# Kernel tuning notes

Hardware: AMD Instinct MI355X
Metric: run time of the kernel (lower is better)

Reference implementation:

```python
import jax, jax.numpy as jnp
import numpy as np
from jax import lax

NEG = jnp.float32(-1e30)  # log-domain 'zero'
BLANK = 0


def setup_inputs() -> dict:
    T, N, C, S = 512, 512, 80, 128
    k0, k1, k2, k3 = jax.random.split(jax.random.key(0), 4)
    logits = jax.random.normal(k0, (T, N, C), dtype=jnp.float32)
    log_probs = jax.nn.log_softmax(logits, axis=-1)  # CTCLoss expects log-probs
    targets = jax.random.randint(k1, (N, S), 1, C).astype(jnp.int32)  # labels in [1, C-1], blank=0 excluded
    input_lengths = jax.random.randint(k2, (N,), T // 2, T + 1).astype(jnp.int32)
    target_lengths = jax.random.randint(k3, (N,), S // 2, S + 1).astype(jnp.int32)
    return {"log_probs": log_probs, "targets": targets,
            "input_lengths": input_lengths, "target_lengths": target_lengths}


def _ctc_loss(log_probs, targets, input_lengths, target_lengths):
    # log_probs: (T, N, C) log-probabilities; targets: (N, S) labels (no blanks)
    T, N, C = log_probs.shape
    S = targets.shape[1]
    L = 2 * S + 1  # extended label length: blank-interleaved

    # extended targets: [blank, y1, blank, y2, ..., yS, blank]  -> (N, L)
    ext = jnp.zeros((N, L), jnp.int32).at[:, 1::2].set(targets)
    # skip transition (s-2 -> s) allowed only if ext[s] != ext[s-2]
    # (blank positions have ext[s]==ext[s-2]==blank, so this also forbids blank skips)
    skip_ok = jnp.pad(ext[:, 2:] != ext[:, :-2], ((0, 0), (2, 0)), constant_values=False)

    # emission log-probs on the lattice: (T, N, L)
    emit = jnp.take_along_axis(log_probs, jnp.broadcast_to(ext[None], (T, N, L)), axis=2)

    # alpha at t=0: only lattice positions 0 (blank) and 1 (first label) reachable
    alpha0 = jnp.full((N, L), NEG).at[:, 0].set(emit[0, :, 0]).at[:, 1].set(emit[0, :, 1])

    def step(alpha, xs):
        em, t = xs  # em: (N, L)
        a1 = jnp.pad(alpha[:, :-1], ((0, 0), (1, 0)), constant_values=NEG)
        a2 = jnp.where(skip_ok,
                       jnp.pad(alpha[:, :-2], ((0, 0), (2, 0)), constant_values=NEG), NEG)
        m = jnp.maximum(alpha, jnp.maximum(a1, a2))
        lse = m + jnp.log(jnp.exp(alpha - m) + jnp.exp(a1 - m) + jnp.exp(a2 - m))
        new = lse + em
        # freeze alpha for finished sequences (t >= input_length)
        alpha_new = jnp.where((t < input_lengths)[:, None], new, alpha)
        return alpha_new, None

    alpha_T, _ = lax.scan(step, alpha0, (emit[1:], jnp.arange(1, T, dtype=jnp.int32)))

    # final states: last blank (2*tl) and last label (2*tl - 1)
    i1 = (2 * target_lengths)[:, None]
    v1 = jnp.take_along_axis(alpha_T, i1, axis=1)[:, 0]
    v2 = jnp.take_along_axis(alpha_T, i1 - 1, axis=1)[:, 0]
    m = jnp.maximum(v1, v2)
    loss = -(m + jnp.log(jnp.exp(v1 - m) + jnp.exp(v2 - m)))
    # zero_infinity=True: infeasible alignments -> 0 loss
    loss = jnp.where(jnp.isfinite(loss) & (loss < 1e10), loss, 0.0)
    return loss  # (N,) reduction='none'


def reference(log_probs, targets, input_lengths, target_lengths):
    return _ctc_loss(log_probs, targets, input_lengths, target_lengths)
```

## Files before the change

### kernel.cpp

```cpp
#include <hip/hip_runtime.h>


#define NEGC  (-1.0e30f)
#define LOG2E 1.4426950408889634f
#define LN2   0.6931471805599453f

constexpr int T_ = 512;
constexpr int C_ = 80;
constexpr int S_ = 128;
constexpr int U_ = 8;
constexpr int WROW = 520;

__device__ __forceinline__ float exp2a(float x) { return __builtin_amdgcn_exp2f(x); }
__device__ __forceinline__ float log2a(float x) { return __builtin_amdgcn_logf(x); }

template <int CTRL>
__device__ __forceinline__ float dppf(float old_, float src) {
    return __int_as_float(__builtin_amdgcn_update_dpp(
        __float_as_int(old_), __float_as_int(src), CTRL, 0xF, 0xF, false));
}

__device__ __forceinline__ int wave_max_bits(float m) {
    m = fmaxf(m, dppf<0x111>(m, m));
    m = fmaxf(m, dppf<0x112>(m, m));
    m = fmaxf(m, dppf<0x114>(m, m));
    m = fmaxf(m, dppf<0x118>(m, m));
    m = fmaxf(m, dppf<0x142>(m, m));
    m = fmaxf(m, dppf<0x143>(m, m));
    return __builtin_amdgcn_readlane(__float_as_int(m), 63);
}

__device__ __forceinline__ float lse2(float x, float y) {
    float m = fmaxf(x, y);
    return m + log2a(1.0f + exp2a(-fabsf(x - y)));
}
__device__ __forceinline__ float lse3(float x, float y, float z) {
    float m = fmaxf(x, fmaxf(y, z));
    return m + log2a(exp2a(x - m) + exp2a(y - m) + exp2a(z - m));
}

__global__ __launch_bounds__(64, 1) void ctc_half(
    const float* __restrict__ lp, const int* __restrict__ tgt,
    const int* __restrict__ ilen, const int* __restrict__ tlen,
    float* __restrict__ ws, int N)
{
    const int b   = blockIdx.x;
    const int n   = b >> 1;
    const int dir = b & 1;
    const int l   = threadIdx.x;

    __shared__ float lds[1280];

    float* ga = ws + (size_t)n * WROW;
    float* gg = ga + 260;

    const int* tn = tgt + n * S_;
    const int ext1 = tn[2 * l];
    const int ext3 = tn[2 * l + 1];
    const int prev = (l > 0) ? tn[2 * l - 1] : 0;
    const bool skip1 = (l > 0) && (ext1 != prev);
    const bool skip3 = (ext3 != ext1);
    const bool skb3  = (l < 63) && (tn[2 * l + 2] != ext3);
    const float k1f  = skip1 ? 1.0f : 0.0f;
    const float k3f  = skip3 ? 1.0f : 0.0f;
    const float kb3f = skb3  ? 1.0f : 0.0f;

    int len = ilen[n];
    len = len < 1 ? 1 : (len > T_ ? T_ : len);
    const int mid = len >> 1;

    const int irst = N * C_;
    const float* lpn = lp + (size_t)n * C_;

    int dkr[10], ckk[10];
    #pragma unroll
    for (int k = 0; k < 10; ++k) {
        const unsigned flat = (unsigned)l + 64u * k;
        const unsigned dk = flat / 80u;
        ckk[k] = (int)(flat - 80u * dk);
        dkr[k] = (int)dk * irst;
    }

    float VA[10], VB[10];
    float ebA[8], e1A[8], e3A[8];
    float ebB[8], e1B[8], e3B[8];

#define SISSUE_F(FB, V) do {                                                   \
    const int s_ = (FB) * irst;                                                \
    _Pragma("unroll")                                                          \
    for (int k = 0; k < 10; ++k)                                               \
        V[k] = lpn[(unsigned)(s_ + dkr[k] + ckk[k])];                          \
} while (0)

#define SISSUE_B(FB, V) do {                                                   \
    const int s_ = (FB) * irst;                                                \
    _Pragma("unroll")                                                          \
    for (int k = 0; k < 10; ++k) {                                             \
        int v_ = s_ - dkr[k]; v_ = v_ < 0 ? 0 : v_;                            \
        V[k] = lpn[(unsigned)(v_ + ckk[k])];                                   \
    }                                                                          \
} while (0)

#define SWRITE(H, V) do {                                                      \
    _Pragma("unroll")                                                          \
    for (int k = 0; k < 10; ++k)                                               \
        lds[(H) * 640 + l + 64 * k] = exp2a(V[k] * LOG2E);                     \
} while (0)

#define RLOAD(H, EB, E1, E3) do {                                              \
    _Pragma("unroll")                                                          \
    for (int u = 0; u < 8; ++u) {                                              \
        const int base_ = (H) * 640 + u * 80;                                  \
        EB[u] = lds[base_];                                                    \
        E1[u] = lds[base_ + ext1];                                             \
        E3[u] = lds[base_ + ext3];                                             \
    }                                                                          \
} while (0)

#define RENORM(S0, S1, S2, S3, S4) do {                                        \
    const int mi_ = wave_max_bits(                                             \
        fmaxf(fmaxf(fmaxf(S0, S1), fmaxf(S2, S3)), S4));                       \
    const int e_ = (mi_ > 0) ? (((mi_ >> 23) & 255) - 187) : 0;                \
    E += e_;                                                                   \
    S0 = ldexpf(S0, -e_); S1 = ldexpf(S1, -e_); S2 = ldexpf(S2, -e_);          \
    S3 = ldexpf(S3, -e_); S4 = ldexpf(S4, -e_);                                \
} while (0)

#define COMP8_F(TB, CEB, CE1, CE3, RH, NEB, NE1, NE3) do {                     \
    _Pragma("unroll")                                                          \
    for (int u = 0; u < 8; ++u) {                                              \
        const int t_ = (TB) + u;                                               \
        const int rb_ = (RH) * 640 + u * 80;                                   \
        NEB[u] = lds[rb_]; NE1[u] = lds[rb_ + ext1]; NE3[u] = lds[rb_ + ext3]; \
        if (t_ < mid) {                                                        \
            const float Pb_ = CEB[u], Q1_ = CE1[u], Q3_ = CE3[u];              \
            const float sm1_ = dppf<0x138>(0.0f, p3_);      \
            const float i0_ = p0_ + sm1_;                                      \
            const float i1_ = fmaf(sm1_, k1f, p1_ + p0_);                      \
            const float i2_ = p2_ + p1_;                                       \
            const float i3_ = fmaf(p1_, k3f, p3_ + p2_);                       \
            const float i4_ = p4_ + p3_;                                       \
            p0_ = i0_ * Pb_; p1_ = i1_ * Q1_; p2_ = i2_ * Pb_;                 \
            p3_ = i3_ * Q3_; p4_ = i4_ * Pb_;                                  \
        }                                                                      \
    }                                                                          \
} while (0)

#define COMP8_B(TB, CEB, CE1, CE3, RH, NEB, NE1, NE3) do {                     \
    _Pragma("unroll")                                                          \
    for (int u = 0; u < 8; ++u) {                                              \
        const int t_ = (TB) - u;                                               \
        const int rb_ = (RH) * 640 + u * 80;                                   \
        NEB[u] = lds[rb_]; NE1[u] = lds[rb_ + ext1]; NE3[u] = lds[rb_ + ext3]; \
        if (t_ >= mid) {                                                       \
            const float Pb_ = CEB[u], Q1_ = CE1[u], Q3_ = CE3[u];              \
            const float x0_ = dppf<0x130>(g4_, g0_);    \
            const float x1_ = dppf<0x130>(0.f, g1_);    \
            const float i0_ = g0_ + g1_;                                       \
            const float i1_ = fmaf(g3_, k3f, g1_ + g2_);                       \
            const float i2_ = g2_ + g3_;                                       \
            const float i3_ = fmaf(x1_, kb3f, g3_ + x0_);                      \
            g0_ = i0_ * Pb_; g1_ = i1_ * Q1_; g2_ = i2_ * Pb_;                 \
            g3_ = i3_ * Q3_; g4_ = g4_ * Pb_;                                  \
        }                                                                      \
    }                                                                          \
} while (0)

    if (dir == 0) {
        SISSUE_F(1, VA);  SISSUE_F(9, VB);
        SWRITE(0, VA);    SWRITE(1, VB);
        SISSUE_F(17, VA); SISSUE_F(25, VB);
        RLOAD(0, ebA, e1A, e3A);

        float p0_ = 0.f, p1_ = 0.f, p2_ = 0.f, p3_ = 0.f, p4_ = 0.f;
        int   E = -60;
        if (l == 0) {
            p0_ = exp2a(lpn[0] * LOG2E + 60.0f);
            p1_ = exp2a(lpn[ext1] * LOG2E + 60.0f);
        }
        for (int tb = 1; tb < mid; tb += 16) {
            COMP8_F(tb, ebA, e1A, e3A, 1, ebB, e1B, e3B);
            RENORM(p0_, p1_, p2_, p3_, p4_);
            SWRITE(0, VA);
            SISSUE_F(tb + 32, VA);
            COMP8_F(tb + 8, ebB, e1B, e3B, 0, ebA, e1A, e3A);
            RENORM(p0_, p1_, p2_, p3_, p4_);
            SWRITE(1, VB);
            SISSUE_F(tb + 40, VB);
        }
        const float fE = (float)E;
        ga[4 * l + 0] = (p0_ > 0.f) ? fmaxf(log2a(p0_) + fE, NEGC) : NEGC;
        ga[4 * l + 1] = (p1_ > 0.f) ? fmaxf(log2a(p1_) + fE, NEGC) : NEGC;
        ga[4 * l + 2] = (p2_ > 0.f) ? fmaxf(log2a(p2_) + fE, NEGC) : NEGC;
        ga[4 * l + 3] = (p3_ > 0.f) ? fmaxf(log2a(p3_) + fE, NEGC) : NEGC;
        if (l == 63) ga[256] = (p4_ > 0.f) ? fmaxf(log2a(p4_) + fE, NEGC) : NEGC;
    } else {
        const int fe = len - 1;
        SISSUE_B(fe - 1, VA);  SISSUE_B(fe - 9, VB);
        SWRITE(0, VA);         SWRITE(1, VB);
        SISSUE_B(fe - 17, VA); SISSUE_B(fe - 25, VB);
        RLOAD(0, ebA, e1A, e3A);

        const int tl = tlen[n];
        const int sA = 2 * tl, sB = 2 * tl - 1;
        float g0_, g1_, g2_, g3_, g4_;
        int E = -60;
        {
            const unsigned feo = (unsigned)(fe * irst);
            const float ebi = lpn[feo] * LOG2E + 60.0f;
            const float e1i = lpn[feo + ext1] * LOG2E + 60.0f;
            const float e3i = lpn[feo + ext3] * LOG2E + 60.0f;
            const int s0 = 4 * l;
            g0_ = (s0     == sA)                 ? exp2a(ebi) : 0.f;
            g1_ = (s0 + 1 == sA || s0 + 1 == sB) ? exp2a(e1i) : 0.f;
            g2_ = (s0 + 2 == sA)                 ? exp2a(ebi) : 0.f;
            g3_ = (s0 + 3 == sA || s0 + 3 == sB) ? exp2a(e3i) : 0.f;
            g4_ = (l == 63 && 256 == sA)         ? exp2a(ebi) : 0.f;
        }
        for (int tb = fe - 1; tb >= mid; tb -= 16) {
            COMP8_B(tb, ebA, e1A, e3A, 1, ebB, e1B, e3B);
            RENORM(g0_, g1_, g2_, g3_, g4_);
            SWRITE(0, VA);
            SISSUE_B(tb - 32, VA);
            COMP8_B(tb - 8, ebB, e1B, e3B, 0, ebA, e1A, e3A);
            RENORM(g0_, g1_, g2_, g3_, g4_);
            SWRITE(1, VB);
            SISSUE_B(tb - 40, VB);
        }
        const float fE = (float)E;
        gg[4 * l + 0] = (g0_ > 0.f) ? fmaxf(log2a(g0_) + fE, NEGC) : NEGC;
        gg[4 * l + 1] = (g1_ > 0.f) ? fmaxf(log2a(g1_) + fE, NEGC) : NEGC;
        gg[4 * l + 2] = (g2_ > 0.f) ? fmaxf(log2a(g2_) + fE, NEGC) : NEGC;
        gg[4 * l + 3] = (g3_ > 0.f) ? fmaxf(log2a(g3_) + fE, NEGC) : NEGC;
        if (l == 63) gg[256] = (g4_ > 0.f) ? fmaxf(log2a(g4_) + fE, NEGC) : NEGC;
    }
#undef COMP8_F
#undef COMP8_B
#undef SISSUE_F
#undef SISSUE_B
#undef SWRITE
#undef RLOAD
#undef RENORM
}

__global__ __launch_bounds__(64) void ctc_comb(
    const float* __restrict__ ws, const int* __restrict__ tgt,
    const int* __restrict__ ilen, const int* __restrict__ tlen,
    float* __restrict__ out, int N)
{
    const int n = blockIdx.x;
    const int l = threadIdx.x;
    const float* ga = ws + (size_t)n * WROW;
    const float* gg = ga + 260;

    int len = ilen[n];
    len = len < 1 ? 1 : (len > T_ ? T_ : len);
    const int tl = tlen[n];

    if (len == 1) {
        if (l == 0) {
            const float v1 = ga[2 * tl];
            const float v2 = (2 * tl >= 1) ? ga[2 * tl - 1] : NEGC;
            float loss = -lse2(v1, v2) * LN2;
            if (!(loss < 1e10f) || !isfinite(loss)) loss = 0.0f;
            out[n] = loss;
        }
        return;
    }

    const int* tn = tgt + n * S_;
    const int ext1 = tn[2 * l];
    const int ext3 = tn[2 * l + 1];
    const int prev = (l > 0) ? tn[2 * l - 1] : 0;
    const bool skip1 = (l > 0) && (ext1 != prev);
    const bool skip3 = (ext3 != ext1);

    const int s0 = 4 * l;
    const float Am1 = (l > 0) ? ga[s0 - 1] : NEGC;
    const float A0 = ga[s0], A1 = ga[s0 + 1], A2 = ga[s0 + 2], A3 = ga[s0 + 3];
    const float v0 = lse2(A0, Am1)                    + gg[s0];
    const float v1 = lse3(A1, A0, skip1 ? Am1 : NEGC) + gg[s0 + 1];
    const float v2 = lse2(A2, A1)                     + gg[s0 + 2];
    const float v3 = lse3(A3, A2, skip3 ? A1 : NEGC)  + gg[s0 + 3];
    const float v4 = (l == 63) ? (lse2(ga[256], A3) + gg[256]) : NEGC;

    float m = fmaxf(fmaxf(v0, v1), fmaxf(fmaxf(v2, v3), v4));
    float ssum = exp2a(v0 - m) + exp2a(v1 - m) + exp2a(v2 - m)
               + exp2a(v3 - m) + exp2a(v4 - m);
    float M = m;
    #pragma unroll
    for (int d = 1; d < 64; d <<= 1) M = fmaxf(M, __shfl_xor(M, d));
    float r = ssum * exp2a(m - M);
    #pragma unroll
    for (int d = 1; d < 64; d <<= 1) r += __shfl_xor(r, d);
    if (l == 0) {
        float loss = -LN2 * (M + log2a(r));
        if (!(loss < 1e10f) || !isfinite(loss)) loss = 0.0f;
        out[n] = loss;
    }
}

__global__ __launch_bounds__(128) void ctc_fused(
    const float* __restrict__ lp, const int* __restrict__ tgt,
    const int* __restrict__ ilen, const int* __restrict__ tlen,
    float* __restrict__ out, int N)
{
    const int n    = blockIdx.x;
    const int wave = threadIdx.x >> 6;
    const int l    = threadIdx.x & 63;

    __shared__ float ga[2 * S_ + 1];
    __shared__ float gg[2 * S_ + 1];

    const int* tn = tgt + n * S_;
    const int ext1 = tn[2 * l];
    const int ext3 = tn[2 * l + 1];
    const int prev = (l > 0) ? tn[2 * l - 1] : 0;
    const bool skip1 = (l > 0) && (ext1 != prev);
    const bool skip3 = (ext3 != ext1);
    const bool skb1 = (tn[2 * l + 1] != tn[2 * l]);
    const bool skb3 = (l < 63) && (tn[2 * l + 2] != tn[2 * l + 1]);

    int len = ilen[n];
    len = len < 1 ? 1 : (len > T_ ? T_ : len);
    const int mid = len >> 1;

    const size_t rstride = (size_t)N * C_;
    const float* lpn = lp + (size_t)n * C_;
    const float* pB = lpn;
    const float* p1 = lpn + ext1;
    const float* p3 = lpn + ext3;

    float rb[U_], r1[U_], r3[U_];

    if (wave == 0) {
        const int last = mid - 1 > 0 ? mid - 1 : 0;
        #pragma unroll
        for (int u = 0; u < U_; ++u) {
            const int r = u + 1;
            const int rc = r < mid ? r : last;
            const size_t o = (size_t)rc * rstride;
            rb[r & 7] = pB[o]; r1[r & 7] = p1[o]; r3[r & 7] = p3[o];
        }
        float a0 = NEGC, a1 = NEGC, a2 = NEGC, a3 = NEGC, a4 = NEGC;
        {
            const float i0 = pB[0] * LOG2E;
            const float i1 = p1[0] * LOG2E;
            if (l == 0) { a0 = i0; a1 = i1; }
        }
        for (int tb = 1; tb < mid; tb += U_) {
            #pragma unroll
            for (int u = 0; u < U_; ++u) {
                const int t = tb + u;
                const int slot = (1 + u) & 7;
                const float eb = rb[slot] * LOG2E;
                const float e1 = r1[slot] * LOG2E;
                const float e3 = r3[slot] * LOG2E;
                const int rr = t + U_;
                const int rc = rr < mid ? rr : last;
                const size_t o = (size_t)rc * rstride;
                const float nrb = pB[o], nr1 = p1[o], nr3 = p3[o];
                if (t < mid) {
                    const float sm1 = dppf<0x138>(NEGC, a3);
                    const float z1 = skip1 ? sm1 : NEGC;
                    const float z3 = skip3 ? a1  : NEGC;
                    const float n0 = lse2(a0, sm1)    + eb;
                    const float n1 = lse3(a1, a0, z1) + e1;
                    const float n2 = lse2(a2, a1)     + eb;
                    const float n3 = lse3(a3, a2, z3) + e3;
                    const float n4 = lse2(a4, a3)     + eb;
                    a0 = n0; a1 = n1; a2 = n2; a3 = n3; a4 = n4;
                }
                rb[slot] = nrb; r1[slot] = nr1; r3[slot] = nr3;
            }
        }
        ga[4 * l + 0] = a0; ga[4 * l + 1] = a1;
        ga[4 * l + 2] = a2; ga[4 * l + 3] = a3;
        if (l == 63) ga[256] = a4;
    } else {
        const int fe = len - 1;
        #pragma unroll
        for (int u = 0; u < U_; ++u) {
            int rc = fe - 1 - u; if (rc < 0) rc = 0;
            const size_t o = (size_t)rc * rstride;
            rb[u] = pB[o]; r1[u] = p1[o]; r3[u] = p3[o];
        }
        const int tl = tlen[n];
        const int sA = 2 * tl, sB = 2 * tl - 1;
        float g0, g1, g2, g3, g4;
        {
            const size_t o = (size_t)fe * rstride;
            const float ebi = pB[o] * LOG2E;
            const float e1i = p1[o] * LOG2E;
            const float e3i = p3[o] * LOG2E;
            const int s0 = 4 * l;
            g0 = (s0     == sA)                 ? ebi : NEGC;
            g1 = (s0 + 1 == sA || s0 + 1 == sB) ? e1i : NEGC;
            g2 = (s0 + 2 == sA)                 ? ebi : NEGC;
            g3 = (s0 + 3 == sA || s0 + 3 == sB) ? e3i : NEGC;
            g4 = (l == 63 && 256 == sA)         ? ebi : NEGC;
        }
        for (int tb = fe - 1; tb >= mid; tb -= U_) {
            #pragma unroll
            for (int u = 0; u < U_; ++u) {
                const int t = tb - u;
                const int slot = ((fe - 1 - tb) + u) & 7;
                const float eb = rb[slot] * LOG2E;
                const float e1 = r1[slot] * LOG2E;
                const float e3 = r3[slot] * LOG2E;
                int rc = t - U_; if (rc < 0) rc = 0;
                const size_t o = (size_t)rc * rstride;
                const float nrb = pB[o], nr1 = p1[o], nr3 = p3[o];
                if (t >= mid) {
                    const float nx0 = dppf<0x130>(g4,   g0);
                    const float nx1 = dppf<0x130>(NEGC, g1);
                    const float z1 = skb1 ? g3  : NEGC;
                    const float z3 = skb3 ? nx1 : NEGC;
                    const float n0 = lse2(g0, g1)      + eb;
                    const float n1 = lse3(g1, g2, z1)  + e1;
                    const float n2 = lse2(g2, g3)      + eb;
                    const float n3 = lse3(g3, nx0, z3) + e3;
                    const float n4 = g4 + eb;
                    g0 = n0; g1 = n1; g2 = n2; g3 = n3; g4 = n4;
                }
                rb[slot] = nrb; r1[slot] = nr1; r3[slot] = nr3;
            }
        }
        gg[4 * l + 0] = g0; gg[4 * l + 1] = g1;
        gg[4 * l + 2] = g2; gg[4 * l + 3] = g3;
        if (l == 63) gg[256] = g4;
    }

    __syncthreads();

    if (wave == 0) {
        const int tl = tlen[n];
        if (len == 1) {
            if (l == 0) {
                const float v1 = ga[2 * tl];
                const float v2 = (2 * tl >= 1) ? ga[2 * tl - 1] : NEGC;
                float loss = -lse2(v1, v2) * LN2;
                if (!(loss < 1e10f) || !isfinite(loss)) loss = 0.0f;
                out[n] = loss;
            }
            return;
        }
        const int s0 = 4 * l;
        const float Am1 = (l > 0) ? ga[s0 - 1] : NEGC;
        const float A0 = ga[s0], A1 = ga[s0 + 1], A2 = ga[s0 + 2], A3 = ga[s0 + 3];
        const float v0 = lse2(A0, Am1)                    + gg[s0];
        const float v1 = lse3(A1, A0, skip1 ? Am1 : NEGC) + gg[s0 + 1];
        const float v2 = lse2(A2, A1)                     + gg[s0 + 2];
        const float v3 = lse3(A3, A2, skip3 ? A1 : NEGC)  + gg[s0 + 3];
        const float v4 = (l == 63) ? (lse2(ga[256], A3) + gg[256]) : NEGC;

        float m = fmaxf(fmaxf(v0, v1), fmaxf(fmaxf(v2, v3), v4));
        float ssum = exp2a(v0 - m) + exp2a(v1 - m) + exp2a(v2 - m)
                   + exp2a(v3 - m) + exp2a(v4 - m);
        float M = m;
        #pragma unroll
        for (int d = 1; d < 64; d <<= 1) M = fmaxf(M, __shfl_xor(M, d));
        float r = ssum * exp2a(m - M);
        #pragma unroll
        for (int d = 1; d < 64; d <<= 1) r += __shfl_xor(r, d);
        if (l == 0) {
            float loss = -LN2 * (M + log2a(r));
            if (!(loss < 1e10f) || !isfinite(loss)) loss = 0.0f;
            out[n] = loss;
        }
    }
}

extern "C" void kernel_launch(void* const* d_in, const int* in_sizes, int n_in,
                              void* d_out, int out_size, void* d_ws, size_t ws_size,
                              hipStream_t stream) {
    const float* lp  = (const float*)d_in[0];
    const int*   tg  = (const int*)  d_in[1];
    const int*   il  = (const int*)  d_in[2];
    const int*   tl  = (const int*)  d_in[3];
    float*       out = (float*)d_out;
    const int N = in_sizes[2];
    const size_t need = (size_t)N * WROW * sizeof(float);
    if (ws_size >= need) {
        ctc_half<<<2 * N, 64, 0, stream>>>(lp, tg, il, tl, (float*)d_ws, N);
        ctc_comb<<<N, 64, 0, stream>>>((const float*)d_ws, tg, il, tl, out, N);
    } else {
        ctc_fused<<<N, 128, 0, stream>>>(lp, tg, il, tl, out, N);
    }
}
```

Before: 133.1 us.

## Fuse forward/backward halves and combine into one two-wave block per sequence

```diff
diff --git a/kernel.cpp b/kernel.cpp
--- a/kernel.cpp
+++ b/kernel.cpp
@@ -8,8 +8,6 @@
 constexpr int T_ = 512;
 constexpr int C_ = 80;
 constexpr int S_ = 128;
-constexpr int U_ = 8;
-constexpr int WROW = 520;
 
 __device__ __forceinline__ float exp2a(float x) { return __builtin_amdgcn_exp2f(x); }
 __device__ __forceinline__ float log2a(float x) { return __builtin_amdgcn_logf(x); }
@@ -39,20 +37,19 @@
     return m + log2a(exp2a(x - m) + exp2a(y - m) + exp2a(z - m));
 }
 
-__global__ __launch_bounds__(64, 1) void ctc_half(
+__global__ __launch_bounds__(128, 1) void ctc_all(
     const float* __restrict__ lp, const int* __restrict__ tgt,
     const int* __restrict__ ilen, const int* __restrict__ tlen,
-    float* __restrict__ ws, int N)
+    float* __restrict__ out, int N)
 {
-    const int b   = blockIdx.x;
-    const int n   = b >> 1;
-    const int dir = b & 1;
-    const int l   = threadIdx.x;
-
-    __shared__ float lds[1280];
-
-    float* ga = ws + (size_t)n * WROW;
-    float* gg = ga + 260;
+    const int n    = blockIdx.x;
+    const int wave = threadIdx.x >> 6;
+    const int l    = threadIdx.x & 63;
+
+    __shared__ float stg[2560];
+    __shared__ float ga[2 * S_ + 1];
+    __shared__ float gg[2 * S_ + 1];
+    float* ldsw = stg + wave * 1280;
 
     const int* tn = tgt + n * S_;
     const int ext1 = tn[2 * l];
@@ -68,6 +65,7 @@
     int len = ilen[n];
     len = len < 1 ? 1 : (len > T_ ? T_ : len);
     const int mid = len >> 1;
+    const int tl  = tlen[n];
 
     const int irst = N * C_;
     const float* lpn = lp + (size_t)n * C_;
@@ -104,16 +102,16 @@
 #define SWRITE(H, V) do {                                                      \
     _Pragma("unroll")                                                          \
     for (int k = 0; k < 10; ++k)                                               \
-        lds[(H) * 640 + l + 64 * k] = exp2a(V[k] * LOG2E);                     \
+        ldsw[(H) * 640 + l + 64 * k] = exp2a(V[k] * LOG2E);                    \
 } while (0)
 
 #define RLOAD(H, EB, E1, E3) do {                                              \
     _Pragma("unroll")                                                          \
     for (int u = 0; u < 8; ++u) {                                              \
         const int base_ = (H) * 640 + u * 80;                                  \
-        EB[u] = lds[base_];                                                    \
-        E1[u] = lds[base_ + ext1];                                             \
-        E3[u] = lds[base_ + ext3];                                             \
+        EB[u] = ldsw[base_];                                                   \
+        E1[u] = ldsw[base_ + ext1];                                            \
+        E3[u] = ldsw[base_ + ext3];                                            \
     }                                                                          \
 } while (0)
 
@@ -131,7 +129,8 @@
     for (int u = 0; u < 8; ++u) {                                              \
         const int t_ = (TB) + u;                                               \
         const int rb_ = (RH) * 640 + u * 80;                                   \
-        NEB[u] = lds[rb_]; NE1[u] = lds[rb_ + ext1]; NE3[u] = lds[rb_ + ext3]; \
+        NEB[u] = ldsw[rb_]; NE1[u] = ldsw[rb_ + ext1];                         \
+        NE3[u] = ldsw[rb_ + ext3];                                             \
         if (t_ < mid) {                                                        \
             const float Pb_ = CEB[u], Q1_ = CE1[u], Q3_ = CE3[u];              \
             const float sm1_ = dppf<0x138>(0.0f, p3_);      \
@@ -151,7 +150,8 @@
     for (int u = 0; u < 8; ++u) {                                              \
         const int t_ = (TB) - u;                                               \
         const int rb_ = (RH) * 640 + u * 80;                                   \
-        NEB[u] = lds[rb_]; NE1[u] = lds[rb_ + ext1]; NE3[u] = lds[rb_ + ext3]; \
+        NEB[u] = ldsw[rb_]; NE1[u] = ldsw[rb_ + ext1];                         \
+        NE3[u] = ldsw[rb_ + ext3];                                             \
         if (t_ >= mid) {                                                       \
             const float Pb_ = CEB[u], Q1_ = CE1[u], Q3_ = CE3[u];              \
             const float x0_ = dppf<0x130>(g4_, g0_);    \
@@ -166,7 +166,7 @@
     }                                                                          \
 } while (0)
 
-    if (dir == 0) {
+    if (wave == 0) {
         SISSUE_F(1, VA);  SISSUE_F(9, VB);
         SWRITE(0, VA);    SWRITE(1, VB);
         SISSUE_F(17, VA); SISSUE_F(25, VB);
@@ -201,7 +201,6 @@
         SISSUE_B(fe - 17, VA); SISSUE_B(fe - 25, VB);
         RLOAD(0, ebA, e1A, e3A);
 
-        const int tl = tlen[n];
         const int sA = 2 * tl, sB = 2 * tl - 1;
         float g0_, g1_, g2_, g3_, g4_;
         int E = -60;
@@ -241,200 +240,10 @@
 #undef SWRITE
 #undef RLOAD
 #undef RENORM
-}
-
-__global__ __launch_bounds__(64) void ctc_comb(
-    const float* __restrict__ ws, const int* __restrict__ tgt,
-    const int* __restrict__ ilen, const int* __restrict__ tlen,
-    float* __restrict__ out, int N)
-{
-    const int n = blockIdx.x;
-    const int l = threadIdx.x;
-    const float* ga = ws + (size_t)n * WROW;
-    const float* gg = ga + 260;
-
-    int len = ilen[n];
-    len = len < 1 ? 1 : (len > T_ ? T_ : len);
-    const int tl = tlen[n];
-
-    if (len == 1) {
-        if (l == 0) {
-            const float v1 = ga[2 * tl];
-            const float v2 = (2 * tl >= 1) ? ga[2 * tl - 1] : NEGC;
-            float loss = -lse2(v1, v2) * LN2;
-            if (!(loss < 1e10f) || !isfinite(loss)) loss = 0.0f;
-            out[n] = loss;
-        }
-        return;
-    }
-
-    const int* tn = tgt + n * S_;
-    const int ext1 = tn[2 * l];
-    const int ext3 = tn[2 * l + 1];
-    const int prev = (l > 0) ? tn[2 * l - 1] : 0;
-    const bool skip1 = (l > 0) && (ext1 != prev);
-    const bool skip3 = (ext3 != ext1);
-
-    const int s0 = 4 * l;
-    const float Am1 = (l > 0) ? ga[s0 - 1] : NEGC;
-    const float A0 = ga[s0], A1 = ga[s0 + 1], A2 = ga[s0 + 2], A3 = ga[s0 + 3];
-    const float v0 = lse2(A0, Am1)                    + gg[s0];
-    const float v1 = lse3(A1, A0, skip1 ? Am1 : NEGC) + gg[s0 + 1];
-    const float v2 = lse2(A2, A1)                     + gg[s0 + 2];
-    const float v3 = lse3(A3, A2, skip3 ? A1 : NEGC)  + gg[s0 + 3];
-    const float v4 = (l == 63) ? (lse2(ga[256], A3) + gg[256]) : NEGC;
-
-    float m = fmaxf(fmaxf(v0, v1), fmaxf(fmaxf(v2, v3), v4));
-    float ssum = exp2a(v0 - m) + exp2a(v1 - m) + exp2a(v2 - m)
-               + exp2a(v3 - m) + exp2a(v4 - m);
-    float M = m;
-    #pragma unroll
-    for (int d = 1; d < 64; d <<= 1) M = fmaxf(M, __shfl_xor(M, d));
-    float r = ssum * exp2a(m - M);
-    #pragma unroll
-    for (int d = 1; d < 64; d <<= 1) r += __shfl_xor(r, d);
-    if (l == 0) {
-        float loss = -LN2 * (M + log2a(r));
-        if (!(loss < 1e10f) || !isfinite(loss)) loss = 0.0f;
-        out[n] = loss;
-    }
-}
-
-__global__ __launch_bounds__(128) void ctc_fused(
-    const float* __restrict__ lp, const int* __restrict__ tgt,
-    const int* __restrict__ ilen, const int* __restrict__ tlen,
-    float* __restrict__ out, int N)
-{
-    const int n    = blockIdx.x;
-    const int wave = threadIdx.x >> 6;
-    const int l    = threadIdx.x & 63;
-
-    __shared__ float ga[2 * S_ + 1];
-    __shared__ float gg[2 * S_ + 1];
-
-    const int* tn = tgt + n * S_;
-    const int ext1 = tn[2 * l];
-    const int ext3 = tn[2 * l + 1];
-    const int prev = (l > 0) ? tn[2 * l - 1] : 0;
-    const bool skip1 = (l > 0) && (ext1 != prev);
-    const bool skip3 = (ext3 != ext1);
-    const bool skb1 = (tn[2 * l + 1] != tn[2 * l]);
-    const bool skb3 = (l < 63) && (tn[2 * l + 2] != tn[2 * l + 1]);
-
-    int len = ilen[n];
-    len = len < 1 ? 1 : (len > T_ ? T_ : len);
-    const int mid = len >> 1;
-
-    const size_t rstride = (size_t)N * C_;
-    const float* lpn = lp + (size_t)n * C_;
-    const float* pB = lpn;
-    const float* p1 = lpn + ext1;
-    const float* p3 = lpn + ext3;
-
-    float rb[U_], r1[U_], r3[U_];
+
+    __syncthreads();
 
     if (wave == 0) {
-        const int last = mid - 1 > 0 ? mid - 1 : 0;
-        #pragma unroll
-        for (int u = 0; u < U_; ++u) {
-            const int r = u + 1;
-            const int rc = r < mid ? r : last;
-            const size_t o = (size_t)rc * rstride;
-            rb[r & 7] = pB[o]; r1[r & 7] = p1[o]; r3[r & 7] = p3[o];
-        }
-        float a0 = NEGC, a1 = NEGC, a2 = NEGC, a3 = NEGC, a4 = NEGC;
-        {
-            const float i0 = pB[0] * LOG2E;
-            const float i1 = p1[0] * LOG2E;
-            if (l == 0) { a0 = i0; a1 = i1; }
-        }
-        for (int tb = 1; tb < mid; tb += U_) {
-            #pragma unroll
-            for (int u = 0; u < U_; ++u) {
-                const int t = tb + u;
-                const int slot = (1 + u) & 7;
-                const float eb = rb[slot] * LOG2E;
-                const float e1 = r1[slot] * LOG2E;
-                const float e3 = r3[slot] * LOG2E;
-                const int rr = t + U_;
-                const int rc = rr < mid ? rr : last;
-                const size_t o = (size_t)rc * rstride;
-                const float nrb = pB[o], nr1 = p1[o], nr3 = p3[o];
-                if (t < mid) {
-                    const float sm1 = dppf<0x138>(NEGC, a3);
-                    const float z1 = skip1 ? sm1 : NEGC;
-                    const float z3 = skip3 ? a1  : NEGC;
-                    const float n0 = lse2(a0, sm1)    + eb;
-                    const float n1 = lse3(a1, a0, z1) + e1;
-                    const float n2 = lse2(a2, a1)     + eb;
-                    const float n3 = lse3(a3, a2, z3) + e3;
-                    const float n4 = lse2(a4, a3)     + eb;
-                    a0 = n0; a1 = n1; a2 = n2; a3 = n3; a4 = n4;
-                }
-                rb[slot] = nrb; r1[slot] = nr1; r3[slot] = nr3;
-            }
-        }
-        ga[4 * l + 0] = a0; ga[4 * l + 1] = a1;
-        ga[4 * l + 2] = a2; ga[4 * l + 3] = a3;
-        if (l == 63) ga[256] = a4;
-    } else {
-        const int fe = len - 1;
-        #pragma unroll
-        for (int u = 0; u < U_; ++u) {
-            int rc = fe - 1 - u; if (rc < 0) rc = 0;
-            const size_t o = (size_t)rc * rstride;
-            rb[u] = pB[o]; r1[u] = p1[o]; r3[u] = p3[o];
-        }
-        const int tl = tlen[n];
-        const int sA = 2 * tl, sB = 2 * tl - 1;
-        float g0, g1, g2, g3, g4;
-        {
-            const size_t o = (size_t)fe * rstride;
-            const float ebi = pB[o] * LOG2E;
-            const float e1i = p1[o] * LOG2E;
-            const float e3i = p3[o] * LOG2E;
-            const int s0 = 4 * l;
-            g0 = (s0     == sA)                 ? ebi : NEGC;
-            g1 = (s0 + 1 == sA || s0 + 1 == sB) ? e1i : NEGC;
-            g2 = (s0 + 2 == sA)                 ? ebi : NEGC;
-            g3 = (s0 + 3 == sA || s0 + 3 == sB) ? e3i : NEGC;
-            g4 = (l == 63 && 256 == sA)         ? ebi : NEGC;
-        }
-        for (int tb = fe - 1; tb >= mid; tb -= U_) {
-            #pragma unroll
-            for (int u = 0; u < U_; ++u) {
-                const int t = tb - u;
-                const int slot = ((fe - 1 - tb) + u) & 7;
-                const float eb = rb[slot] * LOG2E;
-                const float e1 = r1[slot] * LOG2E;
-                const float e3 = r3[slot] * LOG2E;
-                int rc = t - U_; if (rc < 0) rc = 0;
-                const size_t o = (size_t)rc * rstride;
-                const float nrb = pB[o], nr1 = p1[o], nr3 = p3[o];
-                if (t >= mid) {
-                    const float nx0 = dppf<0x130>(g4,   g0);
-                    const float nx1 = dppf<0x130>(NEGC, g1);
-                    const float z1 = skb1 ? g3  : NEGC;
-                    const float z3 = skb3 ? nx1 : NEGC;
-                    const float n0 = lse2(g0, g1)      + eb;
-                    const float n1 = lse3(g1, g2, z1)  + e1;
-                    const float n2 = lse2(g2, g3)      + eb;
-                    const float n3 = lse3(g3, nx0, z3) + e3;
-                    const float n4 = g4 + eb;
-                    g0 = n0; g1 = n1; g2 = n2; g3 = n3; g4 = n4;
-                }
-                rb[slot] = nrb; r1[slot] = nr1; r3[slot] = nr3;
-            }
-        }
-        gg[4 * l + 0] = g0; gg[4 * l + 1] = g1;
-        gg[4 * l + 2] = g2; gg[4 * l + 3] = g3;
-        if (l == 63) gg[256] = g4;
-    }
-
-    __syncthreads();
-
-    if (wave == 0) {
-        const int tl = tlen[n];
         if (len == 1) {
             if (l == 0) {
                 const float v1 = ga[2 * tl];
@@ -480,11 +289,6 @@
     const int*   tl  = (const int*)  d_in[3];
     float*       out = (float*)d_out;
     const int N = in_sizes[2];
-    const size_t need = (size_t)N * WROW * sizeof(float);
-    if (ws_size >= need) {
-        ctc_half<<<2 * N, 64, 0, stream>>>(lp, tg, il, tl, (float*)d_ws, N);
-        ctc_comb<<<N, 64, 0, stream>>>((const float*)d_ws, tg, il, tl, out, N);
-    } else {
-        ctc_fused<<<N, 128, 0, stream>>>(lp, tg, il, tl, out, N);
-    }
-}
+    (void)d_ws; (void)ws_size;
+    ctc_all<<<N, 128, 0, stream>>>(lp, tg, il, tl, out, N);
+}
```

Result: no change. 133.4 us (+0.3%).
